# Kernel tuning notes

Measured on AMD Instinct MI355X. Metric: run time of the kernel, lower is better.

Reference implementation:

```python
import jax, jax.numpy as jnp
import numpy as np

N_NODES = 200000
N_PATCHES = 256
TIMESTEPS = 12
NHID = 16
HORIZON = 12
IN_DIM = NHID * TIMESTEPS + TIMESTEPS  # 204


def setup_inputs() -> dict:
    key = jax.random.key(0)
    ks = jax.random.split(key, 6)
    mixer_x = jax.random.normal(ks[0], (1, TIMESTEPS, N_PATCHES, NHID), dtype=jnp.float32)
    features = jax.random.normal(ks[1], (N_NODES, TIMESTEPS), dtype=jnp.float32)
    W1 = jax.random.normal(ks[2], (IN_DIM, IN_DIM), dtype=jnp.float32) * (1.0 / np.sqrt(IN_DIM))
    b1 = jnp.zeros((IN_DIM,), dtype=jnp.float32)
    W2 = jax.random.normal(ks[3], (IN_DIM, HORIZON), dtype=jnp.float32) * (1.0 / np.sqrt(IN_DIM))
    b2 = jnp.zeros((HORIZON,), dtype=jnp.float32)
    node_patch = jax.random.randint(ks[4], (N_NODES,), 0, N_PATCHES, dtype=jnp.int32)
    return {"mixer_x": mixer_x, "features": features, "W1": W1, "b1": b1,
            "W2": W2, "b2": b2, "node_patch": node_patch}


def reference(mixer_x, features, W1, b1, W2, b2, node_patch):
    # mixer_x: (b, t, p, f) -> per-patch flattened features 'b p (t f)'
    b, t, p, f = mixer_x.shape
    patch_feat = jnp.transpose(mixer_x, (0, 2, 1, 3)).reshape(b, p, t * f)
    # per-node gather of its patch's features: (b, N, t*f)
    g = jnp.take(patch_feat, node_patch, axis=1)
    # node features broadcast over batch: (b, N, t)
    node_x = jnp.broadcast_to(features[None], (b,) + features.shape)
    x = jnp.concatenate([g, node_x], axis=-1)  # (b, N, in_dim)
    h = jax.nn.relu(jnp.einsum('bni,ij->bnj', x, W1) + b1)
    out = jnp.einsum('bnh,ho->bno', h, W2) + b2  # (1, N, horizon)
    return out
```

## Files before the change

kernel.cpp:

```cpp
#include <hip/hip_runtime.h>
#include <hip/hip_bf16.h>

#define N_NODES   200000
#define N_PATCHES 256
#define TSTEPS    12
#define NHID      16
#define HORIZON   12
#define GDIM      192
#define IN_DIM    204
#define NCHUNKS   6250
#define K2_THREADS 512
#define TOTAL_WAVES 2048

#define TROW_U16  232
#define TROW_U4   29
#define TBL_U4    7424

typedef __attribute__((ext_vector_type(8)))  short        bf16x8;
typedef __attribute__((ext_vector_type(16))) float        f32x16;
typedef __attribute__((ext_vector_type(4)))  unsigned int u32x4;

__device__ __forceinline__ unsigned int pk2(float lo, float hi) {
    unsigned short l = __builtin_bit_cast(unsigned short, __float2bfloat16(lo));
    unsigned short h = __builtin_bit_cast(unsigned short, __float2bfloat16(hi));
    return ((unsigned int)h << 16) | (unsigned int)l;
}

__device__ __forceinline__ unsigned int cvtpk(float lo, float hi) {
    unsigned int r;
    asm("v_cvt_pk_bf16_f32 %0, %1, %2" : "=v"(r) : "v"(lo), "v"(hi));
    return r;
}

__device__ __forceinline__ bf16x8 frag_of(unsigned int a, unsigned int b,
                                          unsigned int c, unsigned int d) {
    u32x4 u; u[0] = a; u[1] = b; u[2] = c; u[3] = d;
    return __builtin_bit_cast(bf16x8, u);
}

__device__ __forceinline__ float bf16bits_lo(unsigned int w) {
    return __builtin_bit_cast(float, w << 16);
}
__device__ __forceinline__ float bf16bits_hi(unsigned int w) {
    return __builtin_bit_cast(float, w & 0xffff0000u);
}

__device__ __forceinline__ void gload_lds16(const uint4* g, uint4* l) {
    __builtin_amdgcn_global_load_lds(
        (const __attribute__((address_space(1))) unsigned int*)g,
        (__attribute__((address_space(3))) unsigned int*)l,
        16, 0, 0);
}

__device__ __forceinline__ float ldW1f(const float* __restrict__ W1, int k, int j) {
    const bool ok = (k < TSTEPS) && (j < IN_DIM);
    const int  idx = ok ? ((GDIM + k) * IN_DIM + j) : 0;
    const float v = W1[idx];
    return ok ? v : 0.0f;
}
__device__ __forceinline__ float ldW2t(const float* __restrict__ W2, int j, int o) {
    const bool ok = (j < IN_DIM) && (o < HORIZON);
    const int  idx = ok ? (j * HORIZON + o) : 0;
    const float v = W2[idx];
    return ok ? v : 0.0f;
}

__device__ __forceinline__ int tiled_idx(int j) {
    const int t = j >> 5, w = j & 31;
    const int G = w >> 3, hb = (w >> 2) & 1, q = w & 3;
    return ((t * 8 + hb * 4 + G) << 2) + q;
}

__global__ __launch_bounds__(1024) void precompute(
    const float* __restrict__ mixer_x,
    const float* __restrict__ W1,
    const float* __restrict__ b1,
    const float* __restrict__ W2,
    unsigned short* __restrict__ patch_t,
    u32x4* __restrict__ wfrag)
{
    const int blk = blockIdx.x;
    const int tid = threadIdx.x;

    if (blk == N_PATCHES) {
        const int lane = tid & 63;
        const int g    = tid >> 6;
        const int jl   = lane & 31;
        const int kb   = 4 * (lane >> 5);
        for (int f = g; f < 20; f += 16) {
            u32x4 u;
            if (f < 7) {
                const int j = f * 32 + jl;
                u[0] = pk2(ldW1f(W1, kb + 0,  j), ldW1f(W1, kb + 1,  j));
                u[1] = pk2(ldW1f(W1, kb + 2,  j), ldW1f(W1, kb + 3,  j));
                u[2] = pk2(ldW1f(W1, kb + 8,  j), ldW1f(W1, kb + 9,  j));
                u[3] = pk2(ldW1f(W1, kb + 10, j), ldW1f(W1, kb + 11, j));
            } else {
                const int j0 = (f - 7) * 16 + kb;
                u[0] = pk2(ldW2t(W2, j0 + 0,  jl), ldW2t(W2, j0 + 1,  jl));
                u[1] = pk2(ldW2t(W2, j0 + 2,  jl), ldW2t(W2, j0 + 3,  jl));
                u[2] = pk2(ldW2t(W2, j0 + 8,  jl), ldW2t(W2, j0 + 9,  jl));
                u[3] = pk2(ldW2t(W2, j0 + 10, jl), ldW2t(W2, j0 + 11, jl));
            }
            wfrag[f * 64 + lane] = u;
        }
        return;
    }

    __shared__ float xs[GDIM];
    __shared__ float partial[3 * IN_DIM];
    const int p = blk;
    const int j = tid & 255;
    const int q = tid >> 8;

    if (tid < GDIM) {
        const int t = tid >> 4, f = tid & 15;
        xs[tid] = mixer_x[(t * N_PATCHES + p) * NHID + f];
    }
    __syncthreads();

    float acc = 0.0f;
    if (j < IN_DIM) {
        acc = (q == 0) ? b1[j] : 0.0f;
        const int ibase = q * 48;
#pragma unroll 16
        for (int i = 0; i < 48; ++i)
            acc = fmaf(xs[ibase + i], W1[(ibase + i) * IN_DIM + j], acc);
        if (q > 0) partial[(q - 1) * IN_DIM + j] = acc;
    }
    __syncthreads();
    if (q == 0) {
        if (j < IN_DIM) {
            const float v = acc + partial[j] + partial[IN_DIM + j] + partial[2 * IN_DIM + j];
            patch_t[p * TROW_U16 + tiled_idx(j)] =
                __builtin_bit_cast(unsigned short, __float2bfloat16(v));
        } else if (j < 224) {
            patch_t[p * TROW_U16 + tiled_idx(j)] = 0;
        }
    }
}

__global__ __launch_bounds__(K2_THREADS) void node_mlp_mfma(
    const float* __restrict__ features,
    const int*   __restrict__ node_patch,
    const unsigned short* __restrict__ patch_t,
    const u32x4* __restrict__ wfrag,
    const float* __restrict__ b2,
    float* __restrict__ out)
{
    __shared__ unsigned short smem[N_PATCHES * TROW_U16];

    const int tid  = threadIdx.x;
    const int lane = tid & 63;
    const int wid  = tid >> 6;
    const int jl   = lane & 31;
    const int hi   = lane >> 5;
    const int hi2  = hi * 2;

    int c = blockIdx.x * 8 + wid;
    float4 fa, fb, fc; int p;
    {
        const float4* fp = (const float4*)(features + (c * 32 + jl) * TSTEPS);
        fa = fp[0]; fb = fp[1]; fc = fp[2];
        p  = node_patch[c * 32 + jl];
    }

    bf16x8 A1f[7], A2f[13];
#pragma unroll
    for (int f = 0; f < 7; ++f)
        A1f[f] = __builtin_bit_cast(bf16x8, wfrag[f * 64 + lane]);
#pragma unroll
    for (int f = 0; f < 13; ++f)
        A2f[f] = __builtin_bit_cast(bf16x8, wfrag[(7 + f) * 64 + lane]);

    const float4 b2A = *(const float4*)(b2 + 4 * hi);
    const float4 b2B = *(const float4*)(b2 + 8);

    {
        const uint4* src = (const uint4*)patch_t;
        uint4* dst = (uint4*)smem;
#pragma unroll
        for (int k = 0; k < 15; ++k) {
            const int i = tid + k * K2_THREADS;
            if (i < TBL_U4) gload_lds16(src + i, dst + i);
        }
    }
    __syncthreads();

    const uint4* ph4 = (const uint4*)smem;

    while (true) {
        const int  cn    = c + TOTAL_WAVES;
        const bool haveN = (cn < NCHUNKS);
        float4 fa2, fb2, fc2; int p2 = 0;
        if (haveN) {
            const float4* fq = (const float4*)(features + (cn * 32 + jl) * TSTEPS);
            fa2 = fq[0]; fb2 = fq[1]; fc2 = fq[2];
            p2  = node_patch[cn * 32 + jl];
        }

        const bf16x8 B1 = frag_of(hi ? cvtpk(fb.x, fb.y) : cvtpk(fa.x, fa.y),
                                  hi ? cvtpk(fb.z, fb.w) : cvtpk(fa.z, fa.w),
                                  hi ? 0u                : cvtpk(fc.x, fc.y),
                                  hi ? 0u                : cvtpk(fc.z, fc.w));

        const int pbase = p * TROW_U4 + hi2;

        f32x16 oE, oO;
#pragma unroll
        for (int e = 0; e < 16; ++e) { oE[e] = 0.0f; oO[e] = 0.0f; }

        uint4 nxa[2], nxb[2];
        nxa[0] = ph4[pbase];
        nxb[0] = ph4[pbase + 1];

#pragma unroll
        for (int t = 0; t < 7; ++t) {
            const uint4 ra = nxa[t & 1];
            const uint4 rb = nxb[t & 1];
            if (t < 6) {
                nxa[(t + 1) & 1] = ph4[pbase + (t + 1) * 4];
                nxb[(t + 1) & 1] = ph4[pbase + (t + 1) * 4 + 1];
            }

            f32x16 acc;
            acc[0]  = bf16bits_lo(ra.x); acc[1]  = bf16bits_hi(ra.x);
            acc[2]  = bf16bits_lo(ra.y); acc[3]  = bf16bits_hi(ra.y);
            acc[4]  = bf16bits_lo(ra.z); acc[5]  = bf16bits_hi(ra.z);
            acc[6]  = bf16bits_lo(ra.w); acc[7]  = bf16bits_hi(ra.w);
            acc[8]  = bf16bits_lo(rb.x); acc[9]  = bf16bits_hi(rb.x);
            acc[10] = bf16bits_lo(rb.y); acc[11] = bf16bits_hi(rb.y);
            acc[12] = bf16bits_lo(rb.z); acc[13] = bf16bits_hi(rb.z);
            acc[14] = bf16bits_lo(rb.w); acc[15] = bf16bits_hi(rb.w);

            acc = __builtin_amdgcn_mfma_f32_32x32x16_bf16(A1f[t], B1, acc, 0, 0, 0);

            const bf16x8 ba = frag_of(
                cvtpk(fmaxf(acc[0], 0.f), fmaxf(acc[1], 0.f)),
                cvtpk(fmaxf(acc[2], 0.f), fmaxf(acc[3], 0.f)),
                cvtpk(fmaxf(acc[4], 0.f), fmaxf(acc[5], 0.f)),
                cvtpk(fmaxf(acc[6], 0.f), fmaxf(acc[7], 0.f)));
            oE = __builtin_amdgcn_mfma_f32_32x32x16_bf16(A2f[2 * t], ba, oE, 0, 0, 0);

            if (t < 6) {
                const bf16x8 bb = frag_of(
                    cvtpk(fmaxf(acc[8],  0.f), fmaxf(acc[9],  0.f)),
                    cvtpk(fmaxf(acc[10], 0.f), fmaxf(acc[11], 0.f)),
                    cvtpk(fmaxf(acc[12], 0.f), fmaxf(acc[13], 0.f)),
                    cvtpk(fmaxf(acc[14], 0.f), fmaxf(acc[15], 0.f)));
                oO = __builtin_amdgcn_mfma_f32_32x32x16_bf16(A2f[2 * t + 1], bb, oO, 0, 0, 0);
            }
        }

        {
            const int node = c * 32 + jl;
            float* orow = out + node * HORIZON;
            const float s0 = oE[0] + oO[0], s1 = oE[1] + oO[1];
            const float s2 = oE[2] + oO[2], s3 = oE[3] + oO[3];
            if (hi == 0) {
                const float s4 = oE[4] + oO[4], s5 = oE[5] + oO[5];
                const float s6 = oE[6] + oO[6], s7 = oE[7] + oO[7];
                *(float4*)(orow + 0) = make_float4(s0 + b2A.x, s1 + b2A.y,
                                                   s2 + b2A.z, s3 + b2A.w);
                *(float4*)(orow + 8) = make_float4(s4 + b2B.x, s5 + b2B.y,
                                                   s6 + b2B.z, s7 + b2B.w);
            } else {
                *(float4*)(orow + 4) = make_float4(s0 + b2A.x, s1 + b2A.y,
                                                   s2 + b2A.z, s3 + b2A.w);
            }
        }

        if (!haveN) break;
        fa = fa2; fb = fb2; fc = fc2; p = p2; c = cn;
    }
}

extern "C" void kernel_launch(void* const* d_in, const int* in_sizes, int n_in,
                              void* d_out, int out_size, void* d_ws, size_t ws_size,
                              hipStream_t stream) {
    const float* mixer_x    = (const float*)d_in[0];
    const float* features   = (const float*)d_in[1];
    const float* W1         = (const float*)d_in[2];
    const float* b1         = (const float*)d_in[3];
    const float* W2         = (const float*)d_in[4];
    const float* b2         = (const float*)d_in[5];
    const int*   node_patch = (const int*)d_in[6];
    float* out = (float*)d_out;

    unsigned short* patch_t = (unsigned short*)d_ws;
    u32x4*          wfrag   = (u32x4*)((char*)d_ws + 118784);

    precompute<<<257, 1024, 0, stream>>>(mixer_x, W1, b1, W2, patch_t, wfrag);

    node_mlp_mfma<<<256, K2_THREADS, 0, stream>>>(features, node_patch,
                                                  patch_t, wfrag, b2, out);
}
```

Before: 23.40 us.

## Fuse precompute and node MLP into one cooperative kernel with grid sync

Merges the per-patch first-layer precompute and the weight-fragment packing into the node MLP kernel, launched cooperatively with 256 blocks. Each block computes one patch's projection with 512 threads instead of 1024, block 0 also packs the weight fragments, and a grid-wide sync separates that phase from the main loop. This removes a second kernel launch and the gap between launches. In exchange it adds grid-sync overhead and cooperative-launch constraints, and the prologue now runs with half the threads per patch.

```diff
diff --git a/kernel.cpp b/kernel.cpp
--- a/kernel.cpp
+++ b/kernel.cpp
@@ -1,5 +1,8 @@
 #include <hip/hip_runtime.h>
 #include <hip/hip_bf16.h>
+#include <hip/hip_cooperative_groups.h>
+
+namespace cg = cooperative_groups;
 
 #define N_NODES   200000
 #define N_PATCHES 256
@@ -71,81 +74,16 @@
     return ((t * 8 + hb * 4 + G) << 2) + q;
 }
 
-__global__ __launch_bounds__(1024) void precompute(
+__global__ __launch_bounds__(K2_THREADS) void fused_mlp(
     const float* __restrict__ mixer_x,
+    const float* __restrict__ features,
     const float* __restrict__ W1,
     const float* __restrict__ b1,
     const float* __restrict__ W2,
+    const float* __restrict__ b2,
+    const int*   __restrict__ node_patch,
     unsigned short* __restrict__ patch_t,
-    u32x4* __restrict__ wfrag)
-{
-    const int blk = blockIdx.x;
-    const int tid = threadIdx.x;
-
-    if (blk == N_PATCHES) {
-        const int lane = tid & 63;
-        const int g    = tid >> 6;
-        const int jl   = lane & 31;
-        const int kb   = 4 * (lane >> 5);
-        for (int f = g; f < 20; f += 16) {
-            u32x4 u;
-            if (f < 7) {
-                const int j = f * 32 + jl;
-                u[0] = pk2(ldW1f(W1, kb + 0,  j), ldW1f(W1, kb + 1,  j));
-                u[1] = pk2(ldW1f(W1, kb + 2,  j), ldW1f(W1, kb + 3,  j));
-                u[2] = pk2(ldW1f(W1, kb + 8,  j), ldW1f(W1, kb + 9,  j));
-                u[3] = pk2(ldW1f(W1, kb + 10, j), ldW1f(W1, kb + 11, j));
-            } else {
-                const int j0 = (f - 7) * 16 + kb;
-                u[0] = pk2(ldW2t(W2, j0 + 0,  jl), ldW2t(W2, j0 + 1,  jl));
-                u[1] = pk2(ldW2t(W2, j0 + 2,  jl), ldW2t(W2, j0 + 3,  jl));
-                u[2] = pk2(ldW2t(W2, j0 + 8,  jl), ldW2t(W2, j0 + 9,  jl));
-                u[3] = pk2(ldW2t(W2, j0 + 10, jl), ldW2t(W2, j0 + 11, jl));
-            }
-            wfrag[f * 64 + lane] = u;
-        }
-        return;
-    }
-
-    __shared__ float xs[GDIM];
-    __shared__ float partial[3 * IN_DIM];
-    const int p = blk;
-    const int j = tid & 255;
-    const int q = tid >> 8;
-
-    if (tid < GDIM) {
-        const int t = tid >> 4, f = tid & 15;
-        xs[tid] = mixer_x[(t * N_PATCHES + p) * NHID + f];
-    }
-    __syncthreads();
-
-    float acc = 0.0f;
-    if (j < IN_DIM) {
-        acc = (q == 0) ? b1[j] : 0.0f;
-        const int ibase = q * 48;
-#pragma unroll 16
-        for (int i = 0; i < 48; ++i)
-            acc = fmaf(xs[ibase + i], W1[(ibase + i) * IN_DIM + j], acc);
-        if (q > 0) partial[(q - 1) * IN_DIM + j] = acc;
-    }
-    __syncthreads();
-    if (q == 0) {
-        if (j < IN_DIM) {
-            const float v = acc + partial[j] + partial[IN_DIM + j] + partial[2 * IN_DIM + j];
-            patch_t[p * TROW_U16 + tiled_idx(j)] =
-                __builtin_bit_cast(unsigned short, __float2bfloat16(v));
-        } else if (j < 224) {
-            patch_t[p * TROW_U16 + tiled_idx(j)] = 0;
-        }
-    }
-}
-
-__global__ __launch_bounds__(K2_THREADS) void node_mlp_mfma(
-    const float* __restrict__ features,
-    const int*   __restrict__ node_patch,
-    const unsigned short* __restrict__ patch_t,
-    const u32x4* __restrict__ wfrag,
-    const float* __restrict__ b2,
+    u32x4* __restrict__ wfrag,
     float* __restrict__ out)
 {
     __shared__ unsigned short smem[N_PATCHES * TROW_U16];
@@ -164,6 +102,67 @@
         fa = fp[0]; fb = fp[1]; fc = fp[2];
         p  = node_patch[c * 32 + jl];
     }
+    const float4 b2A = *(const float4*)(b2 + 4 * hi);
+    const float4 b2B = *(const float4*)(b2 + 8);
+
+    {
+        float* xsf  = (float*)smem;
+        float* part = (float*)smem + 192;
+        const int pa = blockIdx.x;
+        const int j  = tid & 255;
+        const int q  = tid >> 8;
+
+        if (tid < GDIM) {
+            const int t = tid >> 4, f = tid & 15;
+            xsf[tid] = mixer_x[(t * N_PATCHES + pa) * NHID + f];
+        }
+        __syncthreads();
+
+        float acc = 0.0f;
+        if (j < IN_DIM) {
+            acc = (q == 0) ? b1[j] : 0.0f;
+            const int ibase = q * 96;
+#pragma unroll 16
+            for (int i = 0; i < 96; ++i)
+                acc = fmaf(xsf[ibase + i], W1[(ibase + i) * IN_DIM + j], acc);
+            if (q) part[j] = acc;
+        }
+        __syncthreads();
+
+        if (q == 0) {
+            if (j < IN_DIM) {
+                const float v = acc + part[j];
+                patch_t[pa * TROW_U16 + tiled_idx(j)] =
+                    __builtin_bit_cast(unsigned short, __float2bfloat16(v));
+            } else if (j < 224) {
+                patch_t[pa * TROW_U16 + tiled_idx(j)] = 0;
+            }
+        }
+
+        if (blockIdx.x == 0) {
+            const int kb = 4 * hi;
+            for (int f = wid; f < 20; f += 8) {
+                u32x4 u;
+                if (f < 7) {
+                    const int j2 = f * 32 + jl;
+                    u[0] = pk2(ldW1f(W1, kb + 0,  j2), ldW1f(W1, kb + 1,  j2));
+                    u[1] = pk2(ldW1f(W1, kb + 2,  j2), ldW1f(W1, kb + 3,  j2));
+                    u[2] = pk2(ldW1f(W1, kb + 8,  j2), ldW1f(W1, kb + 9,  j2));
+                    u[3] = pk2(ldW1f(W1, kb + 10, j2), ldW1f(W1, kb + 11, j2));
+                } else {
+                    const int j0 = (f - 7) * 16 + kb;
+                    u[0] = pk2(ldW2t(W2, j0 + 0,  jl), ldW2t(W2, j0 + 1,  jl));
+                    u[1] = pk2(ldW2t(W2, j0 + 2,  jl), ldW2t(W2, j0 + 3,  jl));
+                    u[2] = pk2(ldW2t(W2, j0 + 8,  jl), ldW2t(W2, j0 + 9,  jl));
+                    u[3] = pk2(ldW2t(W2, j0 + 10, jl), ldW2t(W2, j0 + 11, jl));
+                }
+                wfrag[f * 64 + lane] = u;
+            }
+        }
+    }
+
+    __threadfence();
+    cg::this_grid().sync();
 
     bf16x8 A1f[7], A2f[13];
 #pragma unroll
@@ -172,9 +171,6 @@
 #pragma unroll
     for (int f = 0; f < 13; ++f)
         A2f[f] = __builtin_bit_cast(bf16x8, wfrag[(7 + f) * 64 + lane]);
-
-    const float4 b2A = *(const float4*)(b2 + 4 * hi);
-    const float4 b2B = *(const float4*)(b2 + 8);
 
     {
         const uint4* src = (const uint4*)patch_t;
@@ -290,8 +286,11 @@
     unsigned short* patch_t = (unsigned short*)d_ws;
     u32x4*          wfrag   = (u32x4*)((char*)d_ws + 118784);
 
-    precompute<<<257, 1024, 0, stream>>>(mixer_x, W1, b1, W2, patch_t, wfrag);
-
-    node_mlp_mfma<<<256, K2_THREADS, 0, stream>>>(features, node_patch,
-                                                  patch_t, wfrag, b2, out);
-}
+    void* args[] = {
+        (void*)&mixer_x, (void*)&features, (void*)&W1, (void*)&b1,
+        (void*)&W2, (void*)&b2, (void*)&node_patch,
+        (void*)&patch_t, (void*)&wfrag, (void*)&out
+    };
+    hipLaunchCooperativeKernel((const void*)fused_mlp, dim3(256),
+                               dim3(K2_THREADS), args, 0, stream);
+}
```

Result: slower. 84.01 us (+259.1%).

## Process two 32-node chunks per wave iteration with interleaved MFMA chains

Applied to the files above, without the earlier changes.

Each wave now handles a pair of 32-node chunks per loop iteration, running two independent MFMA chains (A and B) interleaved for ILP. Even/odd output accumulators are merged into one per chunk, removing the final add. The software prefetch of the next chunk's features and the double-buffered LDS reads are dropped. With 3125 pairs over 2048 waves, most waves do one iteration and the rest two, which can leave the load unbalanced.

```diff
diff --git a/kernel.cpp b/kernel.cpp
--- a/kernel.cpp
+++ b/kernel.cpp
@@ -8,7 +8,7 @@
 #define HORIZON   12
 #define GDIM      192
 #define IN_DIM    204
-#define NCHUNKS   6250
+#define NPAIRS    3125
 #define K2_THREADS 512
 #define TOTAL_WAVES 2048
 
@@ -69,6 +69,13 @@
     const int t = j >> 5, w = j & 31;
     const int G = w >> 3, hb = (w >> 2) & 1, q = w & 3;
     return ((t * 8 + hb * 4 + G) << 2) + q;
+}
+
+__device__ __forceinline__ void expand8(const uint4& r, f32x16& acc, int e0) {
+    acc[e0 + 0] = bf16bits_lo(r.x); acc[e0 + 1] = bf16bits_hi(r.x);
+    acc[e0 + 2] = bf16bits_lo(r.y); acc[e0 + 3] = bf16bits_hi(r.y);
+    acc[e0 + 4] = bf16bits_lo(r.z); acc[e0 + 5] = bf16bits_hi(r.z);
+    acc[e0 + 6] = bf16bits_lo(r.w); acc[e0 + 7] = bf16bits_hi(r.w);
 }
 
 __global__ __launch_bounds__(1024) void precompute(
@@ -157,12 +164,16 @@
     const int hi   = lane >> 5;
     const int hi2  = hi * 2;
 
-    int c = blockIdx.x * 8 + wid;
-    float4 fa, fb, fc; int p;
+    int pr = blockIdx.x * 8 + wid;
+    float4 faA, fbA, fcA, faB, fbB, fcB; int pA, pB;
     {
-        const float4* fp = (const float4*)(features + (c * 32 + jl) * TSTEPS);
-        fa = fp[0]; fb = fp[1]; fc = fp[2];
-        p  = node_patch[c * 32 + jl];
+        const int nA = pr * 64 + jl;
+        const float4* fpA = (const float4*)(features + nA * TSTEPS);
+        const float4* fpB = (const float4*)(features + (nA + 32) * TSTEPS);
+        faA = fpA[0]; fbA = fpA[1]; fcA = fpA[2];
+        faB = fpB[0]; fbB = fpB[1]; fcB = fpB[2];
+        pA  = node_patch[nA];
+        pB  = node_patch[nA + 32];
     }
 
     bf16x8 A1f[7], A2f[13];
@@ -190,88 +201,102 @@
     const uint4* ph4 = (const uint4*)smem;
 
     while (true) {
-        const int  cn    = c + TOTAL_WAVES;
-        const bool haveN = (cn < NCHUNKS);
-        float4 fa2, fb2, fc2; int p2 = 0;
-        if (haveN) {
-            const float4* fq = (const float4*)(features + (cn * 32 + jl) * TSTEPS);
-            fa2 = fq[0]; fb2 = fq[1]; fc2 = fq[2];
-            p2  = node_patch[cn * 32 + jl];
-        }
-
-        const bf16x8 B1 = frag_of(hi ? cvtpk(fb.x, fb.y) : cvtpk(fa.x, fa.y),
-                                  hi ? cvtpk(fb.z, fb.w) : cvtpk(fa.z, fa.w),
-                                  hi ? 0u                : cvtpk(fc.x, fc.y),
-                                  hi ? 0u                : cvtpk(fc.z, fc.w));
-
-        const int pbase = p * TROW_U4 + hi2;
-
-        f32x16 oE, oO;
-#pragma unroll
-        for (int e = 0; e < 16; ++e) { oE[e] = 0.0f; oO[e] = 0.0f; }
-
-        uint4 nxa[2], nxb[2];
-        nxa[0] = ph4[pbase];
-        nxb[0] = ph4[pbase + 1];
+        const bf16x8 B1A = frag_of(hi ? cvtpk(fbA.x, fbA.y) : cvtpk(faA.x, faA.y),
+                                   hi ? cvtpk(fbA.z, fbA.w) : cvtpk(faA.z, faA.w),
+                                   hi ? 0u                  : cvtpk(fcA.x, fcA.y),
+                                   hi ? 0u                  : cvtpk(fcA.z, fcA.w));
+        const bf16x8 B1B = frag_of(hi ? cvtpk(fbB.x, fbB.y) : cvtpk(faB.x, faB.y),
+                                   hi ? cvtpk(fbB.z, fbB.w) : cvtpk(faB.z, faB.w),
+                                   hi ? 0u                  : cvtpk(fcB.x, fcB.y),
+                                   hi ? 0u                  : cvtpk(fcB.z, fcB.w));
+
+        const int pbA = pA * TROW_U4 + hi2;
+        const int pbB = pB * TROW_U4 + hi2;
+
+        f32x16 oA, oB;
+#pragma unroll
+        for (int e = 0; e < 16; ++e) { oA[e] = 0.0f; oB[e] = 0.0f; }
 
 #pragma unroll
         for (int t = 0; t < 7; ++t) {
-            const uint4 ra = nxa[t & 1];
-            const uint4 rb = nxb[t & 1];
+            const uint4 raA = ph4[pbA + t * 4];
+            const uint4 rbA = ph4[pbA + t * 4 + 1];
+            const uint4 raB = ph4[pbB + t * 4];
+            const uint4 rbB = ph4[pbB + t * 4 + 1];
+
+            f32x16 accA, accB;
+            expand8(raA, accA, 0); expand8(rbA, accA, 8);
+            expand8(raB, accB, 0); expand8(rbB, accB, 8);
+
+            accA = __builtin_amdgcn_mfma_f32_32x32x16_bf16(A1f[t], B1A, accA, 0, 0, 0);
+            accB = __builtin_amdgcn_mfma_f32_32x32x16_bf16(A1f[t], B1B, accB, 0, 0, 0);
+
+            const bf16x8 baA = frag_of(
+                cvtpk(fmaxf(accA[0], 0.f), fmaxf(accA[1], 0.f)),
+                cvtpk(fmaxf(accA[2], 0.f), fmaxf(accA[3], 0.f)),
+                cvtpk(fmaxf(accA[4], 0.f), fmaxf(accA[5], 0.f)),
+                cvtpk(fmaxf(accA[6], 0.f), fmaxf(accA[7], 0.f)));
+            const bf16x8 baB = frag_of(
+                cvtpk(fmaxf(accB[0], 0.f), fmaxf(accB[1], 0.f)),
+                cvtpk(fmaxf(accB[2], 0.f), fmaxf(accB[3], 0.f)),
+                cvtpk(fmaxf(accB[4], 0.f), fmaxf(accB[5], 0.f)),
+                cvtpk(fmaxf(accB[6], 0.f), fmaxf(accB[7], 0.f)));
+            oA = __builtin_amdgcn_mfma_f32_32x32x16_bf16(A2f[2 * t], baA, oA, 0, 0, 0);
+            oB = __builtin_amdgcn_mfma_f32_32x32x16_bf16(A2f[2 * t], baB, oB, 0, 0, 0);
+
             if (t < 6) {
-                nxa[(t + 1) & 1] = ph4[pbase + (t + 1) * 4];
-                nxb[(t + 1) & 1] = ph4[pbase + (t + 1) * 4 + 1];
+                const bf16x8 bbA = frag_of(
+                    cvtpk(fmaxf(accA[8],  0.f), fmaxf(accA[9],  0.f)),
+                    cvtpk(fmaxf(accA[10], 0.f), fmaxf(accA[11], 0.f)),
+                    cvtpk(fmaxf(accA[12], 0.f), fmaxf(accA[13], 0.f)),
+                    cvtpk(fmaxf(accA[14], 0.f), fmaxf(accA[15], 0.f)));
+                const bf16x8 bbB = frag_of(
+                    cvtpk(fmaxf(accB[8],  0.f), fmaxf(accB[9],  0.f)),
+                    cvtpk(fmaxf(accB[10], 0.f), fmaxf(accB[11], 0.f)),
+                    cvtpk(fmaxf(accB[12], 0.f), fmaxf(accB[13], 0.f)),
+                    cvtpk(fmaxf(accB[14], 0.f), fmaxf(accB[15], 0.f)));
+                oA = __builtin_amdgcn_mfma_f32_32x32x16_bf16(A2f[2 * t + 1], bbA, oA, 0, 0, 0);
+                oB = __builtin_amdgcn_mfma_f32_32x32x16_bf16(A2f[2 * t + 1], bbB, oB, 0, 0, 0);
             }
-
-            f32x16 acc;
-            acc[0]  = bf16bits_lo(ra.x); acc[1]  = bf16bits_hi(ra.x);
-            acc[2]  = bf16bits_lo(ra.y); acc[3]  = bf16bits_hi(ra.y);
-            acc[4]  = bf16bits_lo(ra.z); acc[5]  = bf16bits_hi(ra.z);
-            acc[6]  = bf16bits_lo(ra.w); acc[7]  = bf16bits_hi(ra.w);
-            acc[8]  = bf16bits_lo(rb.x); acc[9]  = bf16bits_hi(rb.x);
-            acc[10] = bf16bits_lo(rb.y); acc[11] = bf16bits_hi(rb.y);
-            acc[12] = bf16bits_lo(rb.z); acc[13] = bf16bits_hi(rb.z);
-            acc[14] = bf16bits_lo(rb.w); acc[15] = bf16bits_hi(rb.w);
-
-            acc = __builtin_amdgcn_mfma_f32_32x32x16_bf16(A1f[t], B1, acc, 0, 0, 0);
-
-            const bf16x8 ba = frag_of(
-                cvtpk(fmaxf(acc[0], 0.f), fmaxf(acc[1], 0.f)),
-                cvtpk(fmaxf(acc[2], 0.f), fmaxf(acc[3], 0.f)),
-                cvtpk(fmaxf(acc[4], 0.f), fmaxf(acc[5], 0.f)),
-                cvtpk(fmaxf(acc[6], 0.f), fmaxf(acc[7], 0.f)));
-            oE = __builtin_amdgcn_mfma_f32_32x32x16_bf16(A2f[2 * t], ba, oE, 0, 0, 0);
-
-            if (t < 6) {
-                const bf16x8 bb = frag_of(
-                    cvtpk(fmaxf(acc[8],  0.f), fmaxf(acc[9],  0.f)),
-                    cvtpk(fmaxf(acc[10], 0.f), fmaxf(acc[11], 0.f)),
-                    cvtpk(fmaxf(acc[12], 0.f), fmaxf(acc[13], 0.f)),
-                    cvtpk(fmaxf(acc[14], 0.f), fmaxf(acc[15], 0.f)));
-                oO = __builtin_amdgcn_mfma_f32_32x32x16_bf16(A2f[2 * t + 1], bb, oO, 0, 0, 0);
+        }
+
+        {
+            const int nA = pr * 64 + jl;
+            float* orow = out + nA * HORIZON;
+            if (hi == 0) {
+                *(float4*)(orow + 0) = make_float4(oA[0] + b2A.x, oA[1] + b2A.y,
+                                                   oA[2] + b2A.z, oA[3] + b2A.w);
+                *(float4*)(orow + 8) = make_float4(oA[4] + b2B.x, oA[5] + b2B.y,
+                                                   oA[6] + b2B.z, oA[7] + b2B.w);
+            } else {
+                *(float4*)(orow + 4) = make_float4(oA[0] + b2A.x, oA[1] + b2A.y,
+                                                   oA[2] + b2A.z, oA[3] + b2A.w);
             }
         }
-
         {
-            const int node = c * 32 + jl;
-            float* orow = out + node * HORIZON;
-            const float s0 = oE[0] + oO[0], s1 = oE[1] + oO[1];
-            const float s2 = oE[2] + oO[2], s3 = oE[3] + oO[3];
+            const int nB = pr * 64 + 32 + jl;
+            float* orow = out + nB * HORIZON;
             if (hi == 0) {
-                const float s4 = oE[4] + oO[4], s5 = oE[5] + oO[5];
-                const float s6 = oE[6] + oO[6], s7 = oE[7] + oO[7];
-                *(float4*)(orow + 0) = make_float4(s0 + b2A.x, s1 + b2A.y,
-                                                   s2 + b2A.z, s3 + b2A.w);
-                *(float4*)(orow + 8) = make_float4(s4 + b2B.x, s5 + b2B.y,
-                                                   s6 + b2B.z, s7 + b2B.w);
+                *(float4*)(orow + 0) = make_float4(oB[0] + b2A.x, oB[1] + b2A.y,
+                                                   oB[2] + b2A.z, oB[3] + b2A.w);
+                *(float4*)(orow + 8) = make_float4(oB[4] + b2B.x, oB[5] + b2B.y,
+                                                   oB[6] + b2B.z, oB[7] + b2B.w);
             } else {
-                *(float4*)(orow + 4) = make_float4(s0 + b2A.x, s1 + b2A.y,
-                                                   s2 + b2A.z, s3 + b2A.w);
+                *(float4*)(orow + 4) = make_float4(oB[0] + b2A.x, oB[1] + b2A.y,
+                                                   oB[2] + b2A.z, oB[3] + b2A.w);
             }
         }
 
-        if (!haveN) break;
-        fa = fa2; fb = fb2; fc = fc2; p = p2; c = cn;
+        pr += TOTAL_WAVES;
+        if (pr >= NPAIRS) break;
+
+        const int nA = pr * 64 + jl;
+        const float4* fpA = (const float4*)(features + nA * TSTEPS);
+        const float4* fpB = (const float4*)(features + (nA + 32) * TSTEPS);
+        faA = fpA[0]; fbA = fpA[1]; fcA = fpA[2];
+        faB = fpB[0]; fbB = fpB[1]; fcB = fpB[2];
+        pA  = node_patch[nA];
+        pB  = node_patch[nA + 32];
     }
 }
 
```

Result: slower. 25.50 us (+9.0%).
